# Optimization experiments

Measured on AMD Instinct MI355X. Metric: run time of the kernel, lower is better.

The kernel has to match this reference:

```python
import jax, jax.numpy as jnp
import numpy as np

H = 2048      # hidden_size
K = 1024      # bottleneck_size
R = 3         # number of roles
B = 8         # batch
S = 2048      # sequence length
LN_EPS = 1e-5


def setup_inputs() -> dict:
    key = jax.random.key(0)
    ks = jax.random.split(key, 8)
    # torch nn.Linear default init ~ U(-1/sqrt(fan_in), 1/sqrt(fan_in)); scale similarly
    sd_d = 1.0 / np.sqrt(H)
    sd_u = 1.0 / np.sqrt(K)
    return {
        "role": jax.random.randint(ks[0], (B,), 0, R),
        "hidden_states": jax.random.normal(ks[1], (B, S, H), dtype=jnp.float32),
        # stacked per-role adapter params
        "W_down": jax.random.uniform(ks[2], (R, H, K), jnp.float32, -sd_d, sd_d),
        "b_down": jax.random.uniform(ks[3], (R, K), jnp.float32, -sd_d, sd_d),
        "W_up": jax.random.uniform(ks[4], (R, K, H), jnp.float32, -sd_u, sd_u),
        "b_up": jax.random.uniform(ks[5], (R, H), jnp.float32, -sd_u, sd_u),
        "gamma": jnp.ones((R, H), jnp.float32),
        "beta": jnp.zeros((R, H), jnp.float32),
    }


def reference(role, hidden_states, W_down, b_down, W_up, b_up, gamma, beta):
    # gather per-sample adapter params by role id: [B, H, K] etc.
    h = jnp.einsum("bsh,bhk->bsk", hidden_states, W_down[role]) + b_down[role][:, None, :]
    h = jax.nn.gelu(h, approximate=False)  # torch nn.GELU default = exact erf
    u = jnp.einsum("bsk,bkh->bsh", h, W_up[role]) + b_up[role][:, None, :]
    y = hidden_states + u
    # LayerNorm over last dim
    mean = jnp.mean(y, axis=-1, keepdims=True)
    var = jnp.mean(jnp.square(y - mean), axis=-1, keepdims=True)
    yn = (y - mean) * jax.lax.rsqrt(var + LN_EPS)
    return yn * gamma[role][:, None, :] + beta[role][:, None, :]
```

## Files before the change

### kernel.cpp

```cpp
#include <hip/hip_runtime.h>
#include <hip/hip_bf16.h>

#define H 2048
#define K 1024
#define R 3
#define BB 8
#define S 2048

typedef __bf16 bf16x8 __attribute__((ext_vector_type(8)));
typedef float f32x4 __attribute__((ext_vector_type(4)));
typedef unsigned short ushort8 __attribute__((ext_vector_type(8)));

static __device__ __forceinline__ unsigned short f2bf(float f) {
    unsigned int u = __float_as_uint(f);
    u += 0x7FFFu + ((u >> 16) & 1u);
    return (unsigned short)(u >> 16);
}

#define GLOAD_LDS16(g, l)                                                      \
    __builtin_amdgcn_global_load_lds(                                          \
        (const __attribute__((address_space(1))) void*)(g),                    \
        (__attribute__((address_space(3))) void*)(l), 16, 0, 0)

__global__ __launch_bounds__(256) void cvt_hs(const float* __restrict__ in,
                                              unsigned short* __restrict__ out,
                                              int n8) {
    int stride = gridDim.x * blockDim.x;
    for (int i = blockIdx.x * blockDim.x + threadIdx.x; i < n8; i += stride) {
        const float4* p = (const float4*)(in + (size_t)i * 8);
        float4 a = p[0], b = p[1];
        union { unsigned short us[8]; ushort8 v; } o;
        o.us[0] = f2bf(a.x); o.us[1] = f2bf(a.y);
        o.us[2] = f2bf(a.z); o.us[3] = f2bf(a.w);
        o.us[4] = f2bf(b.x); o.us[5] = f2bf(b.y);
        o.us[6] = f2bf(b.z); o.us[7] = f2bf(b.w);
        *(ushort8*)(out + (size_t)i * 8) = o.v;
    }
}

__global__ __launch_bounds__(256) void tpose(const float* __restrict__ in,
                                             unsigned short* __restrict__ out,
                                             int rows, int cols) {
    __shared__ float tile[32][33];
    int rr = blockIdx.z;
    const float* ip = in + (size_t)rr * rows * cols;
    unsigned short* op = out + (size_t)rr * rows * cols;
    int x = blockIdx.x * 32 + threadIdx.x;
    int y0 = blockIdx.y * 32 + threadIdx.y;
#pragma unroll
    for (int j = 0; j < 32; j += 8)
        tile[threadIdx.y + j][threadIdx.x] = ip[(size_t)(y0 + j) * cols + x];
    __syncthreads();
    int ox = blockIdx.y * 32 + threadIdx.x;
    int oy0 = blockIdx.x * 32 + threadIdx.y;
#pragma unroll
    for (int j = 0; j < 32; j += 8)
        op[(size_t)(oy0 + j) * rows + ox] = f2bf(tile[threadIdx.x][threadIdx.y + j]);
}

template <int KC, int EPI>
__global__ __launch_bounds__(512, 2) void gemm_8ph(
    const unsigned short* __restrict__ A, const unsigned short* __restrict__ Bt,
    const int* __restrict__ role, const float* __restrict__ bias,
    const float* __restrict__ resid, void* __restrict__ Out, int N) {
    constexpr int NT = KC / 64;
    __shared__ char smem[131072];
    const int tid = threadIdx.x;
    const int wid = tid >> 6, lane = tid & 63;
    const int wm = wid >> 2, wn = wid & 3;
    const int lr = lane & 15, lc = lane >> 4;

    const int nx = N >> 8;
    const int cpx = gridDim.x >> 3;
    const int orig = (blockIdx.x & 7) * cpx + (blockIdx.x >> 3);
    const int tn = orig % nx;
    const int tmz = orig / nx;
    const int tm = tmz & 7;
    const int z = tmz >> 3;
    const int r = role[z];

    const char* Ab = (const char*)(A + ((size_t)z * S + (size_t)tm * 256) * KC);
    const char* Bb = (const char*)(Bt + ((size_t)r * N + (size_t)tn * 256) * KC);

    const int P16 = tid * 16;

#define STAGE_HALF(gbase, ab, half, slot, kt)                                  \
    do {                                                                       \
        _Pragma("unroll") for (int c_ = 0; c_ < 2; c_++) {                     \
            int P_ = c_ * 8192 + P16;                                          \
            int L_ = P_ ^ (((P_ >> 7) & 7) << 4);                              \
            const char* g_ = (gbase) +                                         \
                (size_t)((half) * 128 + (L_ >> 7)) * (KC * 2) +                \
                (size_t)(kt) * 128 + (L_ & 127);                               \
            GLOAD_LDS16(g_, smem + (slot) * 65536 + (ab) * 32768 +             \
                              (half) * 16384 + P_);                            \
        }                                                                      \
    } while (0)

    STAGE_HALF(Ab, 0, 0, 0, 0);
    STAGE_HALF(Ab, 0, 1, 0, 0);
    STAGE_HALF(Bb, 1, 0, 0, 0);
    STAGE_HALF(Bb, 1, 1, 0, 0);
    STAGE_HALF(Bb, 1, 0, 1, 1);
    STAGE_HALF(Bb, 1, 1, 1, 1);
    asm volatile("s_waitcnt vmcnt(4)" ::: "memory");
    __builtin_amdgcn_s_barrier();

    f32x4 acc[8][4] = {};
    const int swz = (lr & 7) << 4;
    const int ck0 = (lc << 4) ^ swz;
    const int ck1 = (0x40 | (lc << 4)) ^ swz;
    const int aBase = wm * 16384 + lr * 128;
    const int bBase = 32768 + (wn >> 1) * 16384 + ((wn & 1) * 64 + lr) * 128;
    const char* sm = smem;

#define LDA4(ibase, pb)                                                        \
    _Pragma("unroll") for (int i_ = 0; i_ < 4; i_++) {                         \
        a[i_][0] = *(const bf16x8*)(sm + (pb) + aBase + ((ibase) + i_) * 2048 + ck0); \
        a[i_][1] = *(const bf16x8*)(sm + (pb) + aBase + ((ibase) + i_) * 2048 + ck1); }
#define LDB2(jbase, pb)                                                        \
    _Pragma("unroll") for (int j_ = 0; j_ < 2; j_++) {                         \
        b[(jbase) + j_][0] = *(const bf16x8*)(sm + (pb) + bBase + ((jbase) + j_) * 2048 + ck0); \
        b[(jbase) + j_][1] = *(const bf16x8*)(sm + (pb) + bBase + ((jbase) + j_) * 2048 + ck1); }
#define MFMA16(IOFF, JOFF)                                                     \
    _Pragma("unroll") for (int kk = 0; kk < 2; kk++)                           \
    _Pragma("unroll") for (int i_ = 0; i_ < 4; i_++)                           \
    _Pragma("unroll") for (int j_ = 0; j_ < 2; j_++)                           \
        acc[(IOFF) + i_][(JOFF) + j_] = __builtin_amdgcn_mfma_f32_16x16x32_bf16( \
            a[i_][kk], b[(JOFF) + j_][kk], acc[(IOFF) + i_][(JOFF) + j_], 0, 0, 0);
#define PH_MID()                                                               \
    __builtin_amdgcn_s_barrier();                                              \
    asm volatile("s_waitcnt lgkmcnt(0)" ::: "memory");                         \
    __builtin_amdgcn_sched_barrier(0);                                         \
    __builtin_amdgcn_s_setprio(1);
#define PH_END()                                                               \
    __builtin_amdgcn_s_setprio(0);                                             \
    __builtin_amdgcn_s_barrier();

#pragma unroll 1
    for (int t = 0; t < NT; t += 2) {
        bf16x8 a[4][2], b[4][2];
        const bool s2ok = (t + 2 < NT), s3ok = (t + 3 < NT);
        LDA4(0, 0); LDB2(0, 0);
        STAGE_HALF(Ab, 0, 0, 1, t + 1);
        asm volatile("s_waitcnt lgkmcnt(8)" ::: "memory");
        PH_MID(); MFMA16(0, 0); PH_END();
        LDB2(2, 0);
        STAGE_HALF(Ab, 0, 1, 1, t + 1);
        PH_MID(); MFMA16(0, 2); PH_END();
        LDA4(4, 0);
        if (s2ok) STAGE_HALF(Bb, 1, 0, 0, t + 2);
        PH_MID(); MFMA16(4, 0); PH_END();
        if (s2ok) STAGE_HALF(Bb, 1, 1, 0, t + 2);
        PH_MID(); MFMA16(4, 2);
        __builtin_amdgcn_s_setprio(0);
        if (s2ok) asm volatile("s_waitcnt vmcnt(4)" ::: "memory");
        else      asm volatile("s_waitcnt vmcnt(0)" ::: "memory");
        __builtin_amdgcn_s_barrier();
        LDA4(0, 65536); LDB2(0, 65536);
        if (s2ok) STAGE_HALF(Ab, 0, 0, 0, t + 2);
        asm volatile("s_waitcnt lgkmcnt(8)" ::: "memory");
        PH_MID(); MFMA16(0, 0); PH_END();
        LDB2(2, 65536);
        if (s2ok) STAGE_HALF(Ab, 0, 1, 0, t + 2);
        PH_MID(); MFMA16(0, 2); PH_END();
        LDA4(4, 65536);
        if (s3ok) STAGE_HALF(Bb, 1, 0, 1, t + 3);
        PH_MID(); MFMA16(4, 0); PH_END();
        if (s3ok) STAGE_HALF(Bb, 1, 1, 1, t + 3);
        PH_MID(); MFMA16(4, 2);
        __builtin_amdgcn_s_setprio(0);
        if (s2ok) {
            if (s3ok) asm volatile("s_waitcnt vmcnt(4)" ::: "memory");
            else      asm volatile("s_waitcnt vmcnt(0)" ::: "memory");
            __builtin_amdgcn_s_barrier();
        }
    }
#undef STAGE_HALF
#undef LDA4
#undef LDB2
#undef MFMA16
#undef PH_MID
#undef PH_END

    const int base_m = tm * 256 + wm * 128;
    const int base_n = tn * 256 + wn * 64;
    float bn[4];
    const float* bp = bias + (size_t)r * N + base_n;
#pragma unroll
    for (int j = 0; j < 4; j++) bn[j] = bp[j * 16 + lr];

    if (EPI == 0) {
        unsigned short* o = (unsigned short*)Out;
#pragma unroll
        for (int i = 0; i < 8; i++) {
#pragma unroll
            for (int j = 0; j < 4; j++) {
#pragma unroll
                for (int q = 0; q < 4; q++) {
                    size_t grow = (size_t)z * S + base_m + i * 16 + lc * 4 + q;
                    int col = base_n + j * 16 + lr;
                    float x = acc[i][j][q] + bn[j];
                    float g = 0.5f * x * (1.0f + erff(x * 0.70710678118654752f));
                    o[grow * N + col] = f2bf(g);
                }
            }
        }
    } else {
        float* o = (float*)Out;
#pragma unroll
        for (int i = 0; i < 8; i++) {
#pragma unroll
            for (int j = 0; j < 4; j++) {
#pragma unroll
                for (int q = 0; q < 4; q++) {
                    size_t grow = (size_t)z * S + base_m + i * 16 + lc * 4 + q;
                    int col = base_n + j * 16 + lr;
                    float y = acc[i][j][q] + bn[j] + resid[grow * H + col];
                    o[grow * (size_t)N + col] = y;
                }
            }
        }
    }
}

__global__ __launch_bounds__(256) void ln_k(float* __restrict__ y,
                                            const int* __restrict__ role,
                                            const float* __restrict__ gamma,
                                            const float* __restrict__ beta) {
    int row = blockIdx.x;
    int z = row / S;
    int r = role[z];
    float* yp = y + (size_t)row * H;
    int t = threadIdx.x;
    float4 v0 = ((const float4*)yp)[t];
    float4 v1 = ((const float4*)yp)[t + 256];
    float s = v0.x + v0.y + v0.z + v0.w + v1.x + v1.y + v1.z + v1.w;
    float ss = v0.x * v0.x + v0.y * v0.y + v0.z * v0.z + v0.w * v0.w +
               v1.x * v1.x + v1.y * v1.y + v1.z * v1.z + v1.w * v1.w;
#pragma unroll
    for (int o = 32; o; o >>= 1) {
        s += __shfl_down(s, o);
        ss += __shfl_down(ss, o);
    }
    __shared__ float ws_s[4], ws_ss[4];
    int wid = t >> 6, lane = t & 63;
    if (lane == 0) { ws_s[wid] = s; ws_ss[wid] = ss; }
    __syncthreads();
    s = ws_s[0] + ws_s[1] + ws_s[2] + ws_s[3];
    ss = ws_ss[0] + ws_ss[1] + ws_ss[2] + ws_ss[3];
    float mean = s * (1.0f / H);
    float var = ss * (1.0f / H) - mean * mean;
    float rstd = rsqrtf(var + 1e-5f);
    const float4* gp = (const float4*)(gamma + (size_t)r * H);
    const float4* bpv = (const float4*)(beta + (size_t)r * H);
    float4 g0 = gp[t], g1 = gp[t + 256];
    float4 b0 = bpv[t], b1 = bpv[t + 256];
    float4 o0, o1;
    o0.x = (v0.x - mean) * rstd * g0.x + b0.x;
    o0.y = (v0.y - mean) * rstd * g0.y + b0.y;
    o0.z = (v0.z - mean) * rstd * g0.z + b0.z;
    o0.w = (v0.w - mean) * rstd * g0.w + b0.w;
    o1.x = (v1.x - mean) * rstd * g1.x + b1.x;
    o1.y = (v1.y - mean) * rstd * g1.y + b1.y;
    o1.z = (v1.z - mean) * rstd * g1.z + b1.z;
    o1.w = (v1.w - mean) * rstd * g1.w + b1.w;
    ((float4*)yp)[t] = o0;
    ((float4*)yp)[t + 256] = o1;
}

extern "C" void kernel_launch(void* const* d_in, const int* in_sizes, int n_in,
                              void* d_out, int out_size, void* d_ws, size_t ws_size,
                              hipStream_t stream) {
    const int* role = (const int*)d_in[0];
    const float* hs = (const float*)d_in[1];
    const float* Wd = (const float*)d_in[2];
    const float* bd = (const float*)d_in[3];
    const float* Wu = (const float*)d_in[4];
    const float* bu = (const float*)d_in[5];
    const float* gamma = (const float*)d_in[6];
    const float* beta = (const float*)d_in[7];
    float* out = (float*)d_out;

    char* ws = (char*)d_ws;
    unsigned short* hs_bf = (unsigned short*)ws;
    unsigned short* wd_t = (unsigned short*)(ws + 67108864);
    unsigned short* wu_t = (unsigned short*)(ws + 67108864 + 12582912);
    unsigned short* h_ws = (unsigned short*)(ws + 67108864 + 2 * 12582912);

    cvt_hs<<<4096, 256, 0, stream>>>(hs, hs_bf, (BB * S * H) / 8);
    dim3 tb(32, 8);
    tpose<<<dim3(K / 32, H / 32, R), tb, 0, stream>>>(Wd, wd_t, H, K);
    tpose<<<dim3(H / 32, K / 32, R), tb, 0, stream>>>(Wu, wu_t, K, H);
    gemm_8ph<H, 0><<<(K / 256) * 8 * BB, 512, 0, stream>>>(hs_bf, wd_t, role, bd, nullptr, h_ws, K);
    gemm_8ph<K, 1><<<(H / 256) * 8 * BB, 512, 0, stream>>>(h_ws, wu_t, role, bu, hs, out, H);
    ln_k<<<BB * S, 256, 0, stream>>>(out, role, gamma, beta);
}
```

Measured before the change: 280.0 us.

## Fuse LayerNorm stats into up-GEMM epilogue, store bf16 residual sum, triple-buffer A

The up-projection GEMM epilogue now computes per-row partial sums and sums of squares, reduced across waves through LDS, and writes them to a partials buffer. The pre-norm activation is stored as bf16 instead of fp32. A lighter LayerNorm kernel combines the partials and reads the bf16 values, cutting the fp32 read-modify-write traffic of the old LN pass. The main loop also moves to a 160KB LDS layout with three A stages and two B stages. Risks are reduced precision in the stored pre-norm values and lower occupancy from the larger shared-memory footprint.

Result: no change. 276.0 us (-1.4%).

```diff
diff --git a/kernel.cpp b/kernel.cpp
--- a/kernel.cpp
+++ b/kernel.cpp
@@ -62,9 +62,10 @@
 __global__ __launch_bounds__(512, 2) void gemm_8ph(
     const unsigned short* __restrict__ A, const unsigned short* __restrict__ Bt,
     const int* __restrict__ role, const float* __restrict__ bias,
-    const float* __restrict__ resid, void* __restrict__ Out, int N) {
+    const float* __restrict__ resid, void* __restrict__ Out,
+    float2* __restrict__ Part, int N) {
     constexpr int NT = KC / 64;
-    __shared__ char smem[131072];
+    __shared__ char smem[163840];
     const int tid = threadIdx.x;
     const int wid = tid >> 6, lane = tid & 63;
     const int wm = wid >> 2, wn = wid & 3;
@@ -84,7 +85,7 @@
 
     const int P16 = tid * 16;
 
-#define STAGE_HALF(gbase, ab, half, slot, kt)                                  \
+#define STAGE16(gbase, ldsbase, kt, half)                                      \
     do {                                                                       \
         _Pragma("unroll") for (int c_ = 0; c_ < 2; c_++) {                     \
             int P_ = c_ * 8192 + P16;                                          \
@@ -92,36 +93,33 @@
             const char* g_ = (gbase) +                                         \
                 (size_t)((half) * 128 + (L_ >> 7)) * (KC * 2) +                \
                 (size_t)(kt) * 128 + (L_ & 127);                               \
-            GLOAD_LDS16(g_, smem + (slot) * 65536 + (ab) * 32768 +             \
-                              (half) * 16384 + P_);                            \
+            GLOAD_LDS16(g_, (ldsbase) + (half) * 16384 + P_);                  \
         }                                                                      \
     } while (0)
 
-    STAGE_HALF(Ab, 0, 0, 0, 0);
-    STAGE_HALF(Ab, 0, 1, 0, 0);
-    STAGE_HALF(Bb, 1, 0, 0, 0);
-    STAGE_HALF(Bb, 1, 1, 0, 0);
-    STAGE_HALF(Bb, 1, 0, 1, 1);
-    STAGE_HALF(Bb, 1, 1, 1, 1);
-    asm volatile("s_waitcnt vmcnt(4)" ::: "memory");
+    STAGE16(Ab, smem, 0, 0);            STAGE16(Ab, smem, 0, 1);
+    STAGE16(Bb, smem + 98304, 0, 0);    STAGE16(Bb, smem + 98304, 0, 1);
+    STAGE16(Ab, smem + 32768, 1, 0);    STAGE16(Ab, smem + 32768, 1, 1);
+    STAGE16(Bb, smem + 131072, 1, 0);   STAGE16(Bb, smem + 131072, 1, 1);
+    asm volatile("s_waitcnt vmcnt(8)" ::: "memory");
     __builtin_amdgcn_s_barrier();
 
     f32x4 acc[8][4] = {};
     const int swz = (lr & 7) << 4;
     const int ck0 = (lc << 4) ^ swz;
-    const int ck1 = (0x40 | (lc << 4)) ^ swz;
-    const int aBase = wm * 16384 + lr * 128;
-    const int bBase = 32768 + (wn >> 1) * 16384 + ((wn & 1) * 64 + lr) * 128;
+    const int ck1 = ck0 ^ 0x40;
     const char* sm = smem;
 
-#define LDA4(ibase, pb)                                                        \
+#define LDA4(ibase, base_)                                                     \
     _Pragma("unroll") for (int i_ = 0; i_ < 4; i_++) {                         \
-        a[i_][0] = *(const bf16x8*)(sm + (pb) + aBase + ((ibase) + i_) * 2048 + ck0); \
-        a[i_][1] = *(const bf16x8*)(sm + (pb) + aBase + ((ibase) + i_) * 2048 + ck1); }
-#define LDB2(jbase, pb)                                                        \
+        int rb_ = (wm * 128 + ((ibase) + i_) * 16 + lr) << 7;                  \
+        a[i_][0] = *(const bf16x8*)(sm + (base_) + rb_ + ck0);                 \
+        a[i_][1] = *(const bf16x8*)(sm + (base_) + rb_ + ck1); }
+#define LDB2(jbase, base_)                                                     \
     _Pragma("unroll") for (int j_ = 0; j_ < 2; j_++) {                         \
-        b[(jbase) + j_][0] = *(const bf16x8*)(sm + (pb) + bBase + ((jbase) + j_) * 2048 + ck0); \
-        b[(jbase) + j_][1] = *(const bf16x8*)(sm + (pb) + bBase + ((jbase) + j_) * 2048 + ck1); }
+        int rb_ = (wn * 64 + ((jbase) + j_) * 16 + lr) << 7;                   \
+        b[(jbase) + j_][0] = *(const bf16x8*)(sm + 98304 + (base_) + rb_ + ck0); \
+        b[(jbase) + j_][1] = *(const bf16x8*)(sm + 98304 + (base_) + rb_ + ck1); }
 #define MFMA16(IOFF, JOFF)                                                     \
     _Pragma("unroll") for (int kk = 0; kk < 2; kk++)                           \
     _Pragma("unroll") for (int i_ = 0; i_ < 4; i_++)                           \
@@ -137,46 +135,50 @@
     __builtin_amdgcn_s_setprio(0);                                             \
     __builtin_amdgcn_s_barrier();
 
+    int as0 = 0, as1 = 1, as2 = 2;
 #pragma unroll 1
     for (int t = 0; t < NT; t += 2) {
         bf16x8 a[4][2], b[4][2];
-        const bool s2ok = (t + 2 < NT), s3ok = (t + 3 < NT);
-        LDA4(0, 0); LDB2(0, 0);
-        STAGE_HALF(Ab, 0, 0, 1, t + 1);
+        const bool pf = (t + 2) < NT;
+        const int saT = as0 * 32768, saT1 = as1 * 32768;
+        char* stA2 = smem + as2 * 32768;
+        char* stA3 = smem + as0 * 32768;
+        LDA4(0, saT); LDB2(0, 0);
+        if (pf) STAGE16(Ab, stA2, t + 2, 0);
         asm volatile("s_waitcnt lgkmcnt(8)" ::: "memory");
         PH_MID(); MFMA16(0, 0); PH_END();
         LDB2(2, 0);
-        STAGE_HALF(Ab, 0, 1, 1, t + 1);
+        if (pf) STAGE16(Ab, stA2, t + 2, 1);
         PH_MID(); MFMA16(0, 2); PH_END();
-        LDA4(4, 0);
-        if (s2ok) STAGE_HALF(Bb, 1, 0, 0, t + 2);
+        LDA4(4, saT);
+        if (pf) STAGE16(Bb, smem + 98304, t + 2, 0);
         PH_MID(); MFMA16(4, 0); PH_END();
-        if (s2ok) STAGE_HALF(Bb, 1, 1, 0, t + 2);
+        if (pf) STAGE16(Bb, smem + 98304, t + 2, 1);
         PH_MID(); MFMA16(4, 2);
         __builtin_amdgcn_s_setprio(0);
-        if (s2ok) asm volatile("s_waitcnt vmcnt(4)" ::: "memory");
-        else      asm volatile("s_waitcnt vmcnt(0)" ::: "memory");
+        if (pf) asm volatile("s_waitcnt vmcnt(8)" ::: "memory");
+        else    asm volatile("s_waitcnt vmcnt(0)" ::: "memory");
         __builtin_amdgcn_s_barrier();
-        LDA4(0, 65536); LDB2(0, 65536);
-        if (s2ok) STAGE_HALF(Ab, 0, 0, 0, t + 2);
+        LDA4(0, saT1); LDB2(0, 32768);
+        if (pf) STAGE16(Ab, stA3, t + 3, 0);
         asm volatile("s_waitcnt lgkmcnt(8)" ::: "memory");
         PH_MID(); MFMA16(0, 0); PH_END();
-        LDB2(2, 65536);
-        if (s2ok) STAGE_HALF(Ab, 0, 1, 0, t + 2);
+        LDB2(2, 32768);
+        if (pf) STAGE16(Ab, stA3, t + 3, 1);
         PH_MID(); MFMA16(0, 2); PH_END();
-        LDA4(4, 65536);
-        if (s3ok) STAGE_HALF(Bb, 1, 0, 1, t + 3);
+        LDA4(4, saT1);
+        if (pf) STAGE16(Bb, smem + 131072, t + 3, 0);
         PH_MID(); MFMA16(4, 0); PH_END();
-        if (s3ok) STAGE_HALF(Bb, 1, 1, 1, t + 3);
+        if (pf) STAGE16(Bb, smem + 131072, t + 3, 1);
         PH_MID(); MFMA16(4, 2);
         __builtin_amdgcn_s_setprio(0);
-        if (s2ok) {
-            if (s3ok) asm volatile("s_waitcnt vmcnt(4)" ::: "memory");
-            else      asm volatile("s_waitcnt vmcnt(0)" ::: "memory");
+        if (pf) {
+            asm volatile("s_waitcnt vmcnt(8)" ::: "memory");
             __builtin_amdgcn_s_barrier();
         }
+        int t0 = as0; as0 = as2; as2 = as1; as1 = t0;
     }
-#undef STAGE_HALF
+#undef STAGE16
 #undef LDA4
 #undef LDB2
 #undef MFMA16
@@ -207,66 +209,80 @@
             }
         }
     } else {
-        float* o = (float*)Out;
+        unsigned short* o = (unsigned short*)Out;
+        float* pl = (float*)smem;
+        __syncthreads();
 #pragma unroll
         for (int i = 0; i < 8; i++) {
 #pragma unroll
-            for (int j = 0; j < 4; j++) {
-#pragma unroll
-                for (int q = 0; q < 4; q++) {
-                    size_t grow = (size_t)z * S + base_m + i * 16 + lc * 4 + q;
+            for (int q = 0; q < 4; q++) {
+                size_t grow = (size_t)z * S + base_m + i * 16 + lc * 4 + q;
+                float s = 0.f, sq = 0.f;
+#pragma unroll
+                for (int j = 0; j < 4; j++) {
                     int col = base_n + j * 16 + lr;
                     float y = acc[i][j][q] + bn[j] + resid[grow * H + col];
-                    o[grow * (size_t)N + col] = y;
+                    o[grow * (size_t)N + col] = f2bf(y);
+                    s += y; sq += y * y;
+                }
+#pragma unroll
+                for (int off = 1; off < 16; off <<= 1) {
+                    s  += __shfl_xor(s, off);
+                    sq += __shfl_xor(sq, off);
+                }
+                if (lr == 0) {
+                    int rloc = wm * 128 + i * 16 + lc * 4 + q;
+                    pl[wn * 256 + rloc] = s;
+                    pl[(4 + wn) * 256 + rloc] = sq;
                 }
             }
         }
+        __syncthreads();
+        if (tid < 256) {
+            float s  = pl[tid] + pl[256 + tid] + pl[512 + tid] + pl[768 + tid];
+            float sq = pl[1024 + tid] + pl[1280 + tid] + pl[1536 + tid] + pl[1792 + tid];
+            size_t grow = (size_t)z * S + tm * 256 + tid;
+            Part[(size_t)tn * (BB * S) + grow] = make_float2(s, sq);
+        }
     }
 }
 
-__global__ __launch_bounds__(256) void ln_k(float* __restrict__ y,
-                                            const int* __restrict__ role,
-                                            const float* __restrict__ gamma,
-                                            const float* __restrict__ beta) {
+__global__ __launch_bounds__(256) void ln2(const unsigned short* __restrict__ ybf,
+                                           const float2* __restrict__ part,
+                                           const int* __restrict__ role,
+                                           const float* __restrict__ gamma,
+                                           const float* __restrict__ beta,
+                                           float* __restrict__ out) {
     int row = blockIdx.x;
-    int z = row / S;
+    int z = row >> 11;
     int r = role[z];
-    float* yp = y + (size_t)row * H;
-    int t = threadIdx.x;
-    float4 v0 = ((const float4*)yp)[t];
-    float4 v1 = ((const float4*)yp)[t + 256];
-    float s = v0.x + v0.y + v0.z + v0.w + v1.x + v1.y + v1.z + v1.w;
-    float ss = v0.x * v0.x + v0.y * v0.y + v0.z * v0.z + v0.w * v0.w +
-               v1.x * v1.x + v1.y * v1.y + v1.z * v1.z + v1.w * v1.w;
-#pragma unroll
-    for (int o = 32; o; o >>= 1) {
-        s += __shfl_down(s, o);
-        ss += __shfl_down(ss, o);
+    float s = 0.f, ss = 0.f;
+#pragma unroll
+    for (int nb = 0; nb < 8; nb++) {
+        float2 p = part[(size_t)nb * (BB * S) + row];
+        s += p.x; ss += p.y;
     }
-    __shared__ float ws_s[4], ws_ss[4];
-    int wid = t >> 6, lane = t & 63;
-    if (lane == 0) { ws_s[wid] = s; ws_ss[wid] = ss; }
-    __syncthreads();
-    s = ws_s[0] + ws_s[1] + ws_s[2] + ws_s[3];
-    ss = ws_ss[0] + ws_ss[1] + ws_ss[2] + ws_ss[3];
     float mean = s * (1.0f / H);
     float var = ss * (1.0f / H) - mean * mean;
     float rstd = rsqrtf(var + 1e-5f);
+    int t = threadIdx.x;
+    ushort8 yv = ((const ushort8*)(ybf + (size_t)row * H))[t];
     const float4* gp = (const float4*)(gamma + (size_t)r * H);
-    const float4* bpv = (const float4*)(beta + (size_t)r * H);
-    float4 g0 = gp[t], g1 = gp[t + 256];
-    float4 b0 = bpv[t], b1 = bpv[t + 256];
-    float4 o0, o1;
-    o0.x = (v0.x - mean) * rstd * g0.x + b0.x;
-    o0.y = (v0.y - mean) * rstd * g0.y + b0.y;
-    o0.z = (v0.z - mean) * rstd * g0.z + b0.z;
-    o0.w = (v0.w - mean) * rstd * g0.w + b0.w;
-    o1.x = (v1.x - mean) * rstd * g1.x + b1.x;
-    o1.y = (v1.y - mean) * rstd * g1.y + b1.y;
-    o1.z = (v1.z - mean) * rstd * g1.z + b1.z;
-    o1.w = (v1.w - mean) * rstd * g1.w + b1.w;
-    ((float4*)yp)[t] = o0;
-    ((float4*)yp)[t + 256] = o1;
+    const float4* bp = (const float4*)(beta + (size_t)r * H);
+    float4 g0 = gp[2 * t], g1 = gp[2 * t + 1];
+    float4 b0 = bp[2 * t], b1 = bp[2 * t + 1];
+    float yo[8];
+#pragma unroll
+    for (int e = 0; e < 8; e++)
+        yo[e] = (__uint_as_float(((unsigned)yv[e]) << 16) - mean) * rstd;
+    float4 r0, r1;
+    r0.x = yo[0] * g0.x + b0.x; r0.y = yo[1] * g0.y + b0.y;
+    r0.z = yo[2] * g0.z + b0.z; r0.w = yo[3] * g0.w + b0.w;
+    r1.x = yo[4] * g1.x + b1.x; r1.y = yo[5] * g1.y + b1.y;
+    r1.z = yo[6] * g1.z + b1.z; r1.w = yo[7] * g1.w + b1.w;
+    float4* op = (float4*)(out + (size_t)row * H);
+    op[2 * t] = r0;
+    op[2 * t + 1] = r1;
 }
 
 extern "C" void kernel_launch(void* const* d_in, const int* in_sizes, int n_in,
@@ -284,7 +300,9 @@
 
     char* ws = (char*)d_ws;
     unsigned short* hs_bf = (unsigned short*)ws;
+    unsigned short* y_bf = (unsigned short*)ws;
     unsigned short* wd_t = (unsigned short*)(ws + 67108864);
+    float2* part = (float2*)(ws + 67108864);
     unsigned short* wu_t = (unsigned short*)(ws + 67108864 + 12582912);
     unsigned short* h_ws = (unsigned short*)(ws + 67108864 + 2 * 12582912);
 
@@ -292,7 +310,9 @@
     dim3 tb(32, 8);
     tpose<<<dim3(K / 32, H / 32, R), tb, 0, stream>>>(Wd, wd_t, H, K);
     tpose<<<dim3(H / 32, K / 32, R), tb, 0, stream>>>(Wu, wu_t, K, H);
-    gemm_8ph<H, 0><<<(K / 256) * 8 * BB, 512, 0, stream>>>(hs_bf, wd_t, role, bd, nullptr, h_ws, K);
-    gemm_8ph<K, 1><<<(H / 256) * 8 * BB, 512, 0, stream>>>(h_ws, wu_t, role, bu, hs, out, H);
-    ln_k<<<BB * S, 256, 0, stream>>>(out, role, gamma, beta);
-}
+    gemm_8ph<H, 0><<<(K / 256) * 8 * BB, 512, 0, stream>>>(hs_bf, wd_t, role, bd,
+                                                           nullptr, h_ws, nullptr, K);
+    gemm_8ph<K, 1><<<(H / 256) * 8 * BB, 512, 0, stream>>>(h_ws, wu_t, role, bu,
+                                                           hs, y_bf, part, H);
+    ln2<<<BB * S, 256, 0, stream>>>(y_bf, part, role, gamma, beta, out);
+}
```
